# Optimization experiments

Measured on AMD Instinct MI355X. Metric: run time of the kernel, lower is better.

## Reference

```python
import jax, jax.numpy as jnp
import numpy as np

N = 1681  # 41*41, fixed by the /1681 normalization in the original loss
BS = 32

def setup_inputs() -> dict:
    key = jax.random.key(0)
    k1, k2 = jax.random.split(key)
    pred = jax.random.normal(k1, (BS, N, N), dtype=jnp.float32)
    target = jax.random.normal(k2, (BS, N, N), dtype=jnp.float32)
    return {"pred": pred, "target": target}

def _col_scale_by_row_norm(x):
    # no = 1/sqrt(sum_k x[l, j, k]^2)  -> per-row L2 norm reciprocal, shape [bs, N]
    # x @ diag(no) scales COLUMN j by no[j]; replace O(N^2 D) matmul with
    inv_rn = 1.0 / jnp.sqrt(jnp.sum(x * x, axis=2))  # [bs, N]
    return x * inv_rn[:, None, :]

def reference(pred, target):
    bs = pred.shape[0]
    p = _col_scale_by_row_norm(pred)
    t = _col_scale_by_row_norm(target)
    losses = -jnp.sum(p * t, axis=(1, 2))  # [bs]
    return jnp.sum(losses) / bs / 1681.0
```

## Files before the change

### kernel.cpp

```cpp
#include <hip/hip_runtime.h>

#define N 1681
#define BS 32
#define BAND 41
#define NBLOCKS (BS * BAND)
#define THREADS 256
#define NROWS_TOTAL (BS * N)


__global__ __launch_bounds__(THREADS) void zero_kernel(float* __restrict__ dcol) {
  const int idx = blockIdx.x * THREADS + threadIdx.x;
  if (idx < NROWS_TOTAL) dcol[idx] = 0.0f;
}

__global__ __launch_bounds__(THREADS, 2) void pass1_kernel(
    const float* __restrict__ pred,
    const float* __restrict__ targ,
    float* __restrict__ sp,
    float* __restrict__ st,
    float* __restrict__ dcol) {
  __shared__ float dsum[N];

  const int b    = blockIdx.x;
  const int tid  = threadIdx.x;
  const int lane = tid & 63;
  const int wid  = tid >> 6;
  const int l    = b / BAND;
  const long R0  = (long)b * BAND;

  for (int idx = tid; idx < N; idx += THREADS) dsum[idx] = 0.0f;
  __syncthreads();

  const float4* __restrict__ pred4 = (const float4*)pred;
  const float4* __restrict__ targ4 = (const float4*)targ;

  const int h = wid;
  float dprod[7][4];
#pragma unroll
  for (int t2 = 0; t2 < 7; ++t2)
#pragma unroll
    for (int ee = 0; ee < 4; ++ee) dprod[t2][ee] = 0.0f;

  float4 pA[7], tA[7], pB[7], tB[7];

#define LOADROW(PBUF, TBUF, RR) do {                                     \
    const long q_ = ((R0 + (RR)) * (long)N) >> 2;                        \
    _Pragma("unroll")                                                    \
    for (int t2 = 0; t2 < 7; ++t2) {                                     \
      if (t2 < 6 || lane < 37) {                                         \
        const long c_ = q_ + t2 * 64 + lane;                             \
        PBUF[t2] = pred4[c_];                                            \
        TBUF[t2] = targ4[c_];                                            \
      }                                                                  \
    }                                                                    \
  } while (0)

#define COMPROW(PBUF, TBUF, RR) do {                                     \
    const long R_ = R0 + (RR);                                           \
    float psq = 0.0f, tsq = 0.0f;                                        \
    _Pragma("unroll")                                                    \
    for (int t2 = 0; t2 < 7; ++t2) {                                     \
      const float pv[4] = {PBUF[t2].x, PBUF[t2].y, PBUF[t2].z, PBUF[t2].w}; \
      const float tv[4] = {TBUF[t2].x, TBUF[t2].y, TBUF[t2].z, TBUF[t2].w}; \
      if (t2 == 0 || t2 == 6) {                                          \
        const int colb = t2 * 256 + 4 * lane - h;                        \
        _Pragma("unroll")                                                \
        for (int ee = 0; ee < 4; ++ee) {                                 \
          const bool ok = (unsigned)(colb + ee) < (unsigned)N;           \
          const float pm = ok ? pv[ee] : 0.0f;                           \
          const float tm = ok ? tv[ee] : 0.0f;                           \
          psq = fmaf(pm, pm, psq);                                       \
          tsq = fmaf(tm, tm, tsq);                                       \
          dprod[t2][ee] = fmaf(pm, tm, dprod[t2][ee]);                   \
        }                                                                \
      } else {                                                           \
        _Pragma("unroll")                                                \
        for (int ee = 0; ee < 4; ++ee) {                                 \
          psq = fmaf(pv[ee], pv[ee], psq);                               \
          tsq = fmaf(tv[ee], tv[ee], tsq);                               \
          dprod[t2][ee] = fmaf(pv[ee], tv[ee], dprod[t2][ee]);           \
        }                                                                \
      }                                                                  \
    }                                                                    \
    _Pragma("unroll")                                                    \
    for (int off = 32; off > 0; off >>= 1) {                             \
      psq += __shfl_down(psq, off, 64);                                  \
      tsq += __shfl_down(tsq, off, 64);                                  \
    }                                                                    \
    if (lane == 0) { sp[R_] = psq; st[R_] = tsq; }                       \
  } while (0)

  const int rr0 = (wid - (int)(R0 & 3)) & 3;

  int rr = rr0;
  LOADROW(pA, tA, rr);
  for (;;) {
    const int r1 = rr + 4;
    if (r1 < BAND) LOADROW(pB, tB, r1);
    COMPROW(pA, tA, rr);
    if (r1 >= BAND) break;
    const int r2 = r1 + 4;
    if (r2 < BAND) LOADROW(pA, tA, r2);
    COMPROW(pB, tB, r1);
    if (r2 >= BAND) break;
    rr = r2;
  }

#pragma unroll
  for (int t2 = 0; t2 < 7; ++t2)
#pragma unroll
    for (int ee = 0; ee < 4; ++ee) {
      const int col = t2 * 256 + 4 * lane + ee - h;
      if ((unsigned)col < (unsigned)N) atomicAdd(&dsum[col], dprod[t2][ee]);
    }
  __syncthreads();

  for (int idx = tid; idx < N; idx += THREADS)
    atomicAdd(&dcol[(size_t)l * N + idx], dsum[idx]);
}

__global__ __launch_bounds__(THREADS) void fin1_kernel(
    const float* __restrict__ sp,
    const float* __restrict__ st,
    const float* __restrict__ dcol,
    float* __restrict__ bsums) {
  __shared__ double red[4];

  double acc = 0.0;
  for (int g = blockIdx.x * THREADS + threadIdx.x; g < NROWS_TOTAL;
       g += gridDim.x * THREADS) {
    const double s = (double)sp[g] * (double)st[g];
    acc += (double)dcol[g] / sqrt(s);
  }
#pragma unroll
  for (int off = 32; off > 0; off >>= 1) acc += __shfl_down(acc, off, 64);
  const int wid = threadIdx.x >> 6;
  if ((threadIdx.x & 63) == 0) red[wid] = acc;
  __syncthreads();
  if (threadIdx.x == 0)
    bsums[blockIdx.x] = (float)(red[0] + red[1] + red[2] + red[3]);
}

__global__ __launch_bounds__(64) void fin2_kernel(
    const float* __restrict__ bsums, float* __restrict__ out) {
  double acc = (double)bsums[threadIdx.x];
#pragma unroll
  for (int off = 32; off > 0; off >>= 1) acc += __shfl_down(acc, off, 64);
  if (threadIdx.x == 0)
    out[0] = (float)(-acc / ((double)BS * (double)N));
}

extern "C" void kernel_launch(void* const* d_in, const int* in_sizes, int n_in,
                              void* d_out, int out_size, void* d_ws, size_t ws_size,
                              hipStream_t stream) {
  const float* pred = (const float*)d_in[0];
  const float* targ = (const float*)d_in[1];

  float* ws    = (float*)d_ws;
  float* sp    = ws;
  float* st    = ws + (size_t)NROWS_TOTAL;
  float* dcol  = ws + (size_t)2 * NROWS_TOTAL;
  float* bsums = ws + (size_t)3 * NROWS_TOTAL;

  zero_kernel<<<(NROWS_TOTAL + THREADS - 1) / THREADS, THREADS, 0, stream>>>(dcol);
  pass1_kernel<<<NBLOCKS, THREADS, 0, stream>>>(pred, targ, sp, st, dcol);
  fin1_kernel<<<64, THREADS, 0, stream>>>(sp, st, dcol, bsums);
  fin2_kernel<<<1, 64, 0, stream>>>(bsums, (float*)d_out);
}
```

Before: 163.8 us.

## Replace global atomics with per-block partials and drop zero kernel

Each pass1 block now writes its column partial sums to a private slice of a partial buffer, replacing the atomicAdd into a shared per-batch column array. This removes the zeroing kernel launch. fin1 now reduces the 41 band partials per column, runs with 128 blocks, and passes double-precision block sums to fin2. Loads are also made unconditional, with the index clamped to the array bound and 32-bit addressing. The cost is a larger workspace (about 9 MB of partials) and an extra read pass over it in fin1.

```diff
diff --git a/kernel.cpp b/kernel.cpp
--- a/kernel.cpp
+++ b/kernel.cpp
@@ -6,26 +6,21 @@
 #define NBLOCKS (BS * BAND)
 #define THREADS 256
 #define NROWS_TOTAL (BS * N)
+#define MAXC ((BS * N * N) / 4)
 
-
-__global__ __launch_bounds__(THREADS) void zero_kernel(float* __restrict__ dcol) {
-  const int idx = blockIdx.x * THREADS + threadIdx.x;
-  if (idx < NROWS_TOTAL) dcol[idx] = 0.0f;
-}
 
 __global__ __launch_bounds__(THREADS, 2) void pass1_kernel(
     const float* __restrict__ pred,
     const float* __restrict__ targ,
     float* __restrict__ sp,
     float* __restrict__ st,
-    float* __restrict__ dcol) {
+    float* __restrict__ dpart) {
   __shared__ float dsum[N];
 
   const int b    = blockIdx.x;
   const int tid  = threadIdx.x;
   const int lane = tid & 63;
   const int wid  = tid >> 6;
-  const int l    = b / BAND;
   const long R0  = (long)b * BAND;
 
   for (int idx = tid; idx < N; idx += THREADS) dsum[idx] = 0.0f;
@@ -43,15 +38,12 @@
 
   float4 pA[7], tA[7], pB[7], tB[7];
 
-#define LOADROW(PBUF, TBUF, RR) do {                                     \
-    const long q_ = ((R0 + (RR)) * (long)N) >> 2;                        \
+#define LOADROW(PBUF, TBUF, CBASE) do {                                  \
     _Pragma("unroll")                                                    \
     for (int t2 = 0; t2 < 7; ++t2) {                                     \
-      if (t2 < 6 || lane < 37) {                                         \
-        const long c_ = q_ + t2 * 64 + lane;                             \
-        PBUF[t2] = pred4[c_];                                            \
-        TBUF[t2] = targ4[c_];                                            \
-      }                                                                  \
+      const int c_ = min((CBASE) + t2 * 64 + lane, MAXC - 1);            \
+      PBUF[t2] = pred4[c_];                                              \
+      TBUF[t2] = targ4[c_];                                              \
     }                                                                    \
   } while (0)
 
@@ -91,19 +83,22 @@
   } while (0)
 
   const int rr0 = (wid - (int)(R0 & 3)) & 3;
+  const int c0  = (int)(((R0 + rr0) * (long)N) >> 2);
 
   int rr = rr0;
-  LOADROW(pA, tA, rr);
+  int cA = c0;
+  LOADROW(pA, tA, cA);
   for (;;) {
     const int r1 = rr + 4;
-    if (r1 < BAND) LOADROW(pB, tB, r1);
+    if (r1 < BAND) LOADROW(pB, tB, cA + N);
     COMPROW(pA, tA, rr);
     if (r1 >= BAND) break;
     const int r2 = r1 + 4;
-    if (r2 < BAND) LOADROW(pA, tA, r2);
+    if (r2 < BAND) LOADROW(pA, tA, cA + 2 * N);
     COMPROW(pB, tB, r1);
     if (r2 >= BAND) break;
     rr = r2;
+    cA += 2 * N;
   }
 
 #pragma unroll
@@ -116,21 +111,27 @@
   __syncthreads();
 
   for (int idx = tid; idx < N; idx += THREADS)
-    atomicAdd(&dcol[(size_t)l * N + idx], dsum[idx]);
+    dpart[(size_t)b * N + idx] = dsum[idx];
 }
 
 __global__ __launch_bounds__(THREADS) void fin1_kernel(
     const float* __restrict__ sp,
     const float* __restrict__ st,
-    const float* __restrict__ dcol,
-    float* __restrict__ bsums) {
+    const float* __restrict__ dpart,
+    double* __restrict__ bsums) {
   __shared__ double red[4];
 
   double acc = 0.0;
   for (int g = blockIdx.x * THREADS + threadIdx.x; g < NROWS_TOTAL;
        g += gridDim.x * THREADS) {
+    const int l = g / N;
+    const int j = g - l * N;
+    float dv = 0.0f;
+    const float* __restrict__ dp = dpart + (size_t)l * BAND * N + j;
+#pragma unroll 41
+    for (int band = 0; band < BAND; ++band) dv += dp[(size_t)band * N];
     const double s = (double)sp[g] * (double)st[g];
-    acc += (double)dcol[g] / sqrt(s);
+    acc += (double)dv / sqrt(s);
   }
 #pragma unroll
   for (int off = 32; off > 0; off >>= 1) acc += __shfl_down(acc, off, 64);
@@ -138,12 +139,12 @@
   if ((threadIdx.x & 63) == 0) red[wid] = acc;
   __syncthreads();
   if (threadIdx.x == 0)
-    bsums[blockIdx.x] = (float)(red[0] + red[1] + red[2] + red[3]);
+    bsums[blockIdx.x] = red[0] + red[1] + red[2] + red[3];
 }
 
 __global__ __launch_bounds__(64) void fin2_kernel(
-    const float* __restrict__ bsums, float* __restrict__ out) {
-  double acc = (double)bsums[threadIdx.x];
+    const double* __restrict__ bsums, float* __restrict__ out) {
+  double acc = bsums[threadIdx.x] + bsums[threadIdx.x + 64];
 #pragma unroll
   for (int off = 32; off > 0; off >>= 1) acc += __shfl_down(acc, off, 64);
   if (threadIdx.x == 0)
@@ -156,14 +157,13 @@
   const float* pred = (const float*)d_in[0];
   const float* targ = (const float*)d_in[1];
 
-  float* ws    = (float*)d_ws;
-  float* sp    = ws;
-  float* st    = ws + (size_t)NROWS_TOTAL;
-  float* dcol  = ws + (size_t)2 * NROWS_TOTAL;
-  float* bsums = ws + (size_t)3 * NROWS_TOTAL;
+  float* ws     = (float*)d_ws;
+  float* dpart  = ws;
+  float* sp     = ws + (size_t)NBLOCKS * N;
+  float* st     = sp + (size_t)NROWS_TOTAL;
+  double* bsums = (double*)(st + (size_t)NROWS_TOTAL + 32);
 
-  zero_kernel<<<(NROWS_TOTAL + THREADS - 1) / THREADS, THREADS, 0, stream>>>(dcol);
-  pass1_kernel<<<NBLOCKS, THREADS, 0, stream>>>(pred, targ, sp, st, dcol);
-  fin1_kernel<<<64, THREADS, 0, stream>>>(sp, st, dcol, bsums);
+  pass1_kernel<<<NBLOCKS, THREADS, 0, stream>>>(pred, targ, sp, st, dpart);
+  fin1_kernel<<<128, THREADS, 0, stream>>>(sp, st, dpart, bsums);
   fin2_kernel<<<1, 64, 0, stream>>>(bsums, (float*)d_out);
 }
```

New measurement: 164.2 us. Within noise of the previous version (+0.3%).
